# Optimization experiments

Measured on AMD Instinct MI355X. Metric: run time of the kernel, lower is better.

The kernel has to match this reference:

```python
import jax, jax.numpy as jnp
import numpy as np

D_MODEL = 512
N_HEADS = 8
HEAD_DIM = D_MODEL // N_HEADS
B, L, S = 4, 2048, 2048


def setup_inputs() -> dict:
    key = jax.random.key(0)
    ks = jax.random.split(key, 16)
    std = 1.0 / np.sqrt(D_MODEL)
    inp = {
        'queries': jax.random.normal(ks[0], (B, L, D_MODEL), jnp.float32),
        'keys': jax.random.normal(ks[1], (B, S, D_MODEL), jnp.float32),
        'values': jax.random.normal(ks[2], (B, S, D_MODEL), jnp.float32),
        'tau': jax.random.uniform(ks[3], (B,), jnp.float32, 0.5, 1.5),
        'delta': jax.random.normal(ks[4], (B,), jnp.float32) * 0.1,
        'Wq': jax.random.normal(ks[5], (D_MODEL, D_MODEL), jnp.float32) * std,
        'bq': jnp.zeros((D_MODEL,), jnp.float32),
        'Wk': jax.random.normal(ks[6], (D_MODEL, D_MODEL), jnp.float32) * std,
        'bk': jnp.zeros((D_MODEL,), jnp.float32),
        'Wv': jax.random.normal(ks[7], (D_MODEL, D_MODEL), jnp.float32) * std,
        'bv': jnp.zeros((D_MODEL,), jnp.float32),
        'Wo': jax.random.normal(ks[8], (D_MODEL, D_MODEL), jnp.float32) * std,
        'bo': jnp.zeros((D_MODEL,), jnp.float32),
    }
    return inp


def reference(queries, keys, values, tau, delta, Wq, bq, Wk, bk, Wv, bv, Wo, bo):
    Bq, Lq, _ = queries.shape
    Sk = keys.shape[1]
    H, E = N_HEADS, HEAD_DIM
    # projections -> [B, L, H, E]
    q = (queries @ Wq + bq).reshape(Bq, Lq, H, E)
    k = (keys @ Wk + bk).reshape(Bq, Sk, H, E)
    v = (values @ Wv + bv).reshape(Bq, Sk, H, E)
    scale = 1.0 / jnp.sqrt(jnp.float32(E))
    # scores: [B, H, L, S]
    scores = jnp.einsum('blhe,bshe->bhls', q, k)
    scores = scores * tau[:, None, None, None] + delta[:, None, None, None]
    A = jax.nn.softmax(scale * scores, axis=-1)  # dropout is identity in eval
    out = jnp.einsum('bhls,bshd->blhd', A, v).reshape(Bq, Lq, H * E)
    return out @ Wo + bo
```

## Files before the change

### kernel.cpp

```cpp
#include <hip/hip_runtime.h>
#include <stdint.h>

#define NB 4
#define LQ 2048
#define DM 512
#define NH 8
#define EH 64
#define MT (NB*LQ)
#define QBLK 128

typedef __attribute__((ext_vector_type(4)))  float f32x4;
typedef __attribute__((ext_vector_type(8)))  __bf16 bf16x8;
typedef __attribute__((ext_vector_type(8)))  unsigned short u16x8;
typedef __attribute__((ext_vector_type(4)))  float float4_t;
typedef __attribute__((ext_vector_type(2)))  unsigned int u32x2;

static __device__ __forceinline__ unsigned short f2bf(float f) {
  unsigned int u = __builtin_bit_cast(unsigned int, f);
  u += 0x7fffu + ((u >> 16) & 1u);
  return (unsigned short)(u >> 16);
}

static __device__ __forceinline__ void gload16(const void* g, void* l) {
  __builtin_amdgcn_global_load_lds(
      (__attribute__((address_space(1))) unsigned int*)(g),
      (__attribute__((address_space(3))) unsigned int*)(l), 16, 0, 0);
}

static __device__ __forceinline__ unsigned int cvt_pk_bf16(float lo, float hi) {
  unsigned int r;
  asm("v_cvt_pk_bf16_f32 %0, %1, %2" : "=v"(r) : "v"(lo), "v"(hi));
  return r;
}

extern "C" __global__ __launch_bounds__(256) void k_cast_x(
    const float* __restrict__ q, const float* __restrict__ k,
    const float* __restrict__ v, unsigned short* __restrict__ x) {
  int z = blockIdx.y;
  const float* src = (z == 0) ? q : ((z == 1) ? k : v);
  unsigned short* dst = x + (size_t)z * MT * DM;
  size_t i = ((size_t)blockIdx.x * 256 + threadIdx.x) * 8;
  float4_t a = *(const float4_t*)(src + i);
  float4_t b = *(const float4_t*)(src + i + 4);
  u16x8 r;
  r[0]=f2bf(a[0]); r[1]=f2bf(a[1]); r[2]=f2bf(a[2]); r[3]=f2bf(a[3]);
  r[4]=f2bf(b[0]); r[5]=f2bf(b[1]); r[6]=f2bf(b[2]); r[7]=f2bf(b[3]);
  *(u16x8*)(dst + i) = r;
}

extern "C" __global__ __launch_bounds__(256) void k_cast_wt(
    const float* __restrict__ wq, const float* __restrict__ wk,
    const float* __restrict__ wv, const float* __restrict__ wo,
    unsigned short* __restrict__ wt) {
  __shared__ float tile[64][65];
  int z = blockIdx.z;
  const float* w = (z==0)?wq : (z==1)?wk : (z==2)?wv : wo;
  unsigned short* dst = wt + (size_t)z * DM * DM;
  int kb = blockIdx.y * 64, nb = blockIdx.x * 64;
  int t = threadIdx.x;
  int r = t >> 2, c0 = (t & 3) * 16;
  #pragma unroll
  for (int i = 0; i < 16; i += 4) {
    float4_t v4 = *(const float4_t*)(w + (size_t)(kb + r) * DM + nb + c0 + i);
    tile[r][c0+i]   = v4[0]; tile[r][c0+i+1] = v4[1];
    tile[r][c0+i+2] = v4[2]; tile[r][c0+i+3] = v4[3];
  }
  __syncthreads();
  u16x8 o0, o1;
  #pragma unroll
  for (int i = 0; i < 8; ++i) o0[i] = f2bf(tile[c0+i][r]);
  #pragma unroll
  for (int i = 0; i < 8; ++i) o1[i] = f2bf(tile[c0+8+i][r]);
  *(u16x8*)(dst + (size_t)(nb + r) * DM + kb + c0)     = o0;
  *(u16x8*)(dst + (size_t)(nb + r) * DM + kb + c0 + 8) = o1;
}

extern "C" __global__ __launch_bounds__(256) void k_gemm_qkv(
    const unsigned short* __restrict__ X, const unsigned short* __restrict__ WT,
    const float* __restrict__ bq, const float* __restrict__ bk,
    const float* __restrict__ bv, unsigned short* __restrict__ out) {
  int z = blockIdx.z;
  const unsigned short* A  = X  + (size_t)z * MT * DM;
  const unsigned short* Bt = WT + (size_t)z * DM * DM;
  const float* bias = (z==0)?bq : (z==1)?bk : bv;
  unsigned short* dst = out + (size_t)z * MT * DM;

  __shared__ unsigned short As[2][128][32];
  __shared__ unsigned short Bs[2][128][32];

  int m0 = blockIdx.y * 128;
  int n0 = blockIdx.x * 128;
  int t = threadIdx.x;
  int lane = t & 63;
  int w = t >> 6;
  int wr = w >> 1, wc = w & 1;
  int g = lane >> 4, r15 = lane & 15;

  f32x4 acc[4][4];
  #pragma unroll
  for (int i=0;i<4;i++)
    #pragma unroll
    for (int j=0;j<4;j++)
      #pragma unroll
      for (int e=0;e<4;e++) acc[i][j][e] = 0.f;

  auto stage = [&](int bb, int kt) {
    int k0 = kt * 32;
    int sblk = (t & 3) ^ ((t >> 3) & 3);
    #pragma unroll
    for (int j=0;j<2;j++) {
      int o = t*16 + j*4096;
      int row = o >> 6;
      gload16(A  + (size_t)(m0+row)*DM + k0 + sblk*8, (char*)(&As[bb][0][0]) + o);
      gload16(Bt + (size_t)(n0+row)*DM + k0 + sblk*8, (char*)(&Bs[bb][0][0]) + o);
    }
  };

  stage(0, 0);
  __syncthreads();
  int buf = 0;
  for (int kt = 0; kt < DM/32; ++kt) {
    if (kt + 1 < DM/32) stage(buf ^ 1, kt + 1);
    bf16x8 af[4], bfr[4];
    #pragma unroll
    for (int mi=0;mi<4;mi++) {
      int row = wr*64 + mi*16 + r15;
      int blk = g ^ ((row >> 1) & 3);
      af[mi] = *(const bf16x8*)(&As[buf][row][blk*8]);
    }
    #pragma unroll
    for (int ni=0;ni<4;ni++) {
      int row = wc*64 + ni*16 + r15;
      int blk = g ^ ((row >> 1) & 3);
      bfr[ni] = *(const bf16x8*)(&Bs[buf][row][blk*8]);
    }
    #pragma unroll
    for (int mi=0;mi<4;mi++)
      #pragma unroll
      for (int ni=0;ni<4;ni++)
        acc[mi][ni] = __builtin_amdgcn_mfma_f32_16x16x32_bf16(af[mi], bfr[ni], acc[mi][ni], 0, 0, 0);
    __syncthreads();
    buf ^= 1;
  }
  #pragma unroll
  for (int ni=0;ni<4;ni++) {
    int n = n0 + wc*64 + ni*16 + r15;
    float bia = bias[n];
    int h = n >> 6, e = n & 63;
    #pragma unroll
    for (int mi=0;mi<4;mi++) {
      #pragma unroll
      for (int rg=0;rg<4;rg++) {
        int m = m0 + wr*64 + mi*16 + g*4 + rg;
        int b = m >> 11, s = m & 2047;
        dst[((size_t)((b*NH + h)*LQ + s))*EH + e] = f2bf(acc[mi][ni][rg] + bia);
      }
    }
  }
}

extern "C" __global__ __launch_bounds__(256) void k_vt(
    const unsigned short* __restrict__ qkv, unsigned short* __restrict__ vtg) {
  __shared__ unsigned short tile[64][65];
  int bh = blockIdx.y;
  int s0 = blockIdx.x * 64;
  const unsigned short* Vh = qkv + (size_t)2*MT*DM + (size_t)bh*LQ*EH;
  unsigned short* Ot = vtg + (size_t)bh*EH*LQ;
  int t = threadIdx.x;
  int r = t >> 2, c0 = (t & 3) * 16;
  u16x8 a = *(const u16x8*)(Vh + (size_t)(s0 + r)*EH + c0);
  u16x8 b = *(const u16x8*)(Vh + (size_t)(s0 + r)*EH + c0 + 8);
  #pragma unroll
  for (int i=0;i<8;i++) { tile[r][c0+i] = a[i]; tile[r][c0+8+i] = b[i]; }
  __syncthreads();
  u16x8 o0, o1;
  #pragma unroll
  for (int i=0;i<8;i++) o0[i] = tile[c0+i][r];
  #pragma unroll
  for (int i=0;i<8;i++) o1[i] = tile[c0+8+i][r];
  *(u16x8*)(Ot + (size_t)r*LQ + s0 + c0)     = o0;
  *(u16x8*)(Ot + (size_t)r*LQ + s0 + c0 + 8) = o1;
}

template<int NSPLIT>
__global__ __launch_bounds__(256, 4) void k_flash(
    const unsigned short* __restrict__ qkv, const unsigned short* __restrict__ vtg,
    const float* __restrict__ tau, unsigned short* __restrict__ aout,
    float* __restrict__ opart, float* __restrict__ lpart) {
  constexpr int SKV = LQ / NSPLIT;
  constexpr int NIT = SKV / 32;
  constexpr int CPX = (512 * NSPLIT) / 8;
  int bid = blockIdx.x;
  int wgid = (bid & 7) * CPX + (bid >> 3);
  int half = wgid % NSPLIT;
  int rest = wgid / NSPLIT;
  int qblk = rest & 15;
  int bh = rest >> 4;
  int batch = bh >> 3, h = bh & 7;

  const unsigned short* Qh  = qkv + (size_t)bh * LQ * EH + (size_t)qblk * QBLK * EH;
  const unsigned short* Kh  = qkv + (size_t)MT * DM + (size_t)bh * LQ * EH + (size_t)half * SKV * EH;
  const unsigned short* VTh = vtg + (size_t)bh * EH * LQ + (size_t)half * SKV;

  __shared__ unsigned short Ks[2][32][64];
  __shared__ unsigned short Vt[2][64][32];
  __shared__ unsigned short Pall[4][32][40];

  int t = threadIdx.x;
  int lane = t & 63;
  int wv = t >> 6;
  int q4 = lane & 15;
  int g  = lane >> 4;
  float C2 = tau[batch] * 0.18033688011112042f;

  unsigned short (*Pw)[40] = Pall[wv];

  auto stage = [&](int bb, int it) {
    int o = t * 16;
    int krow = t >> 3;
    int sblk = (t & 7) ^ ((krow ^ (krow >> 3)) & 7);
    gload16(Kh + (size_t)(it*32 + krow)*EH + sblk*8, (char*)(&Ks[bb][0][0]) + o);
    gload16(VTh + (size_t)(t >> 2)*LQ + it*32 + (t & 3)*8, (char*)(&Vt[bb][0][0]) + o);
  };

  bf16x8 qf[2][2];
  #pragma unroll
  for (int qt=0;qt<2;qt++)
    #pragma unroll
    for (int st=0;st<2;st++)
      qf[qt][st] = *(const bf16x8*)(Qh + (size_t)(wv*32 + qt*16 + q4)*EH + st*32 + g*8);

  stage(0, 0);

  const f32x4 Z4 = {0.f, 0.f, 0.f, 0.f};
  f32x4 oacc[4][2];
  #pragma unroll
  for (int a=0;a<4;a++)
    #pragma unroll
    for (int b2=0;b2<2;b2++)
      #pragma unroll
      for (int e=0;e<4;e++) oacc[a][b2][e] = 0.f;
  float lsp[2] = {0.f, 0.f};

  __syncthreads();
  int buf = 0;
  for (int it = 0; it < NIT; ++it) {
    if (it + 1 < NIT) stage(buf ^ 1, it + 1);

    f32x4 sac[2][2];
    __builtin_amdgcn_s_setprio(1);
    #pragma unroll
    for (int kvt=0; kvt<2; ++kvt) {
      int row = kvt*16 + q4;
      int S = (row ^ (row >> 3)) & 7;
      bf16x8 kf0 = *(const bf16x8*)(&Ks[buf][row][(g ^ S)*8]);
      sac[kvt][0] = __builtin_amdgcn_mfma_f32_16x16x32_bf16(kf0, qf[0][0], Z4, 0,0,0);
      sac[kvt][1] = __builtin_amdgcn_mfma_f32_16x16x32_bf16(kf0, qf[1][0], Z4, 0,0,0);
    }
    #pragma unroll
    for (int kvt=0; kvt<2; ++kvt) {
      int row = kvt*16 + q4;
      int S = (row ^ (row >> 3)) & 7;
      bf16x8 kf1 = *(const bf16x8*)(&Ks[buf][row][((4 + g) ^ S)*8]);
      sac[kvt][0] = __builtin_amdgcn_mfma_f32_16x16x32_bf16(kf1, qf[0][1], sac[kvt][0], 0,0,0);
      sac[kvt][1] = __builtin_amdgcn_mfma_f32_16x16x32_bf16(kf1, qf[1][1], sac[kvt][1], 0,0,0);
    }
    __builtin_amdgcn_s_setprio(0);

    #pragma unroll
    for (int qt=0; qt<2; ++qt) {
      int qrow = qt*16 + q4;
      #pragma unroll
      for (int kvt=0; kvt<2; ++kvt) {
        float p0 = __builtin_amdgcn_exp2f(sac[kvt][qt][0] * C2);
        float p1 = __builtin_amdgcn_exp2f(sac[kvt][qt][1] * C2);
        float p2 = __builtin_amdgcn_exp2f(sac[kvt][qt][2] * C2);
        float p3 = __builtin_amdgcn_exp2f(sac[kvt][qt][3] * C2);
        lsp[qt] += (p0 + p1) + (p2 + p3);
        u32x2 wpk;
        wpk[0] = cvt_pk_bf16(p0, p1);
        wpk[1] = cvt_pk_bf16(p2, p3);
        *(u32x2*)(&Pw[qrow][kvt*16 + g*4]) = wpk;
      }
    }
    asm volatile("s_waitcnt lgkmcnt(0)" ::: "memory");
    __builtin_amdgcn_sched_barrier(0);

    bf16x8 pf[2];
    #pragma unroll
    for (int qt=0; qt<2; ++qt)
      pf[qt] = *(const bf16x8*)(&Pw[qt*16 + q4][g*8]);
    __builtin_amdgcn_s_setprio(1);
    #pragma unroll
    for (int et=0; et<4; ++et) {
      bf16x8 vf = *(const bf16x8*)(&Vt[buf][et*16 + q4][g*8]);
      oacc[et][0] = __builtin_amdgcn_mfma_f32_16x16x32_bf16(vf, pf[0], oacc[et][0], 0,0,0);
      oacc[et][1] = __builtin_amdgcn_mfma_f32_16x16x32_bf16(vf, pf[1], oacc[et][1], 0,0,0);
    }
    __builtin_amdgcn_s_setprio(0);

    __syncthreads();
    buf ^= 1;
  }

  #pragma unroll
  for (int qt=0; qt<2; ++qt) {
    float s = lsp[qt];
    s += __shfl_xor(s, 16, 64);
    s += __shfl_xor(s, 32, 64);
    int q = qblk*QBLK + wv*32 + qt*16 + q4;
    if constexpr (NSPLIT == 1) {
      float inv = 1.f / s;
      unsigned short* rowp = aout + (size_t)(batch*LQ + q)*DM + h*EH;
      #pragma unroll
      for (int et=0; et<4; ++et) {
        #pragma unroll
        for (int rg=0; rg<4; rg+=2) {
          int e = et*16 + g*4 + rg;
          *(unsigned int*)(rowp + e) = cvt_pk_bf16(oacc[et][qt][rg] * inv, oacc[et][qt][rg+1] * inv);
        }
      }
    } else {
      size_t r = (size_t)bh * LQ + q;
      float* od = opart + (r*NSPLIT + half) * 64;
      #pragma unroll
      for (int et=0; et<4; ++et)
        *(float4_t*)(od + et*16 + g*4) = oacc[et][qt];
      if (g == 0) lpart[r*NSPLIT + half] = s;
    }
  }
}

extern "C" __global__ __launch_bounds__(256) void k_red(
    const float* __restrict__ op, const float* __restrict__ lp,
    unsigned short* __restrict__ aout) {
  int t = threadIdx.x;
  int r = blockIdx.x * 16 + (t >> 4);
  int e0 = (t & 15) * 4;
  float4_t a = *(const float4_t*)(op + ((size_t)r*2)*64 + e0);
  float4_t b = *(const float4_t*)(op + ((size_t)r*2 + 1)*64 + e0);
  float inv = 1.f / (lp[(size_t)r*2] + lp[(size_t)r*2 + 1]);
  int bh = r >> 11, q = r & 2047, batch = bh >> 3, h = bh & 7;
  unsigned short* dst = aout + (size_t)(batch*LQ + q)*DM + h*EH + e0;
  u32x2 w;
  w[0] = cvt_pk_bf16((a[0]+b[0])*inv, (a[1]+b[1])*inv);
  w[1] = cvt_pk_bf16((a[2]+b[2])*inv, (a[3]+b[3])*inv);
  *(u32x2*)dst = w;
}

extern "C" __global__ __launch_bounds__(256) void k_gemm_out(
    const unsigned short* __restrict__ A, const unsigned short* __restrict__ WT,
    const float* __restrict__ bo, float* __restrict__ out) {
  const unsigned short* Bt = WT + (size_t)3 * DM * DM;

  __shared__ unsigned short As[2][128][32];
  __shared__ unsigned short Bs[2][128][32];

  int m0 = blockIdx.y * 128;
  int n0 = blockIdx.x * 128;
  int t = threadIdx.x;
  int lane = t & 63;
  int w = t >> 6;
  int wr = w >> 1, wc = w & 1;
  int g = lane >> 4, r15 = lane & 15;

  f32x4 acc[4][4];
  #pragma unroll
  for (int i=0;i<4;i++)
    #pragma unroll
    for (int j=0;j<4;j++)
      #pragma unroll
      for (int e=0;e<4;e++) acc[i][j][e] = 0.f;

  auto stage = [&](int bb, int kt) {
    int k0 = kt * 32;
    int sblk = (t & 3) ^ ((t >> 3) & 3);
    #pragma unroll
    for (int j=0;j<2;j++) {
      int o = t*16 + j*4096;
      int row = o >> 6;
      gload16(A  + (size_t)(m0+row)*DM + k0 + sblk*8, (char*)(&As[bb][0][0]) + o);
      gload16(Bt + (size_t)(n0+row)*DM + k0 + sblk*8, (char*)(&Bs[bb][0][0]) + o);
    }
  };

  stage(0, 0);
  __syncthreads();
  int buf = 0;
  for (int kt = 0; kt < DM/32; ++kt) {
    if (kt + 1 < DM/32) stage(buf ^ 1, kt + 1);
    bf16x8 af[4], bfr[4];
    #pragma unroll
    for (int mi=0;mi<4;mi++) {
      int row = wr*64 + mi*16 + r15;
      int blk = g ^ ((row >> 1) & 3);
      af[mi] = *(const bf16x8*)(&As[buf][row][blk*8]);
    }
    #pragma unroll
    for (int ni=0;ni<4;ni++) {
      int row = wc*64 + ni*16 + r15;
      int blk = g ^ ((row >> 1) & 3);
      bfr[ni] = *(const bf16x8*)(&Bs[buf][row][blk*8]);
    }
    #pragma unroll
    for (int mi=0;mi<4;mi++)
      #pragma unroll
      for (int ni=0;ni<4;ni++)
        acc[mi][ni] = __builtin_amdgcn_mfma_f32_16x16x32_bf16(af[mi], bfr[ni], acc[mi][ni], 0, 0, 0);
    __syncthreads();
    buf ^= 1;
  }
  #pragma unroll
  for (int ni=0;ni<4;ni++) {
    int n = n0 + wc*64 + ni*16 + r15;
    float bia = bo[n];
    #pragma unroll
    for (int mi=0;mi<4;mi++) {
      #pragma unroll
      for (int rg=0;rg<4;rg++) {
        int m = m0 + wr*64 + mi*16 + g*4 + rg;
        out[(size_t)m*DM + n] = acc[mi][ni][rg] + bia;
      }
    }
  }
}

extern "C" void kernel_launch(void* const* d_in, const int* in_sizes, int n_in,
                              void* d_out, int out_size, void* d_ws, size_t ws_size,
                              hipStream_t stream) {
  const float* queries = (const float*)d_in[0];
  const float* keys    = (const float*)d_in[1];
  const float* values  = (const float*)d_in[2];
  const float* tau     = (const float*)d_in[3];
  const float* Wq = (const float*)d_in[5];
  const float* bq = (const float*)d_in[6];
  const float* Wk = (const float*)d_in[7];
  const float* bk = (const float*)d_in[8];
  const float* Wv = (const float*)d_in[9];
  const float* bv = (const float*)d_in[10];
  const float* Wo = (const float*)d_in[11];
  const float* bo = (const float*)d_in[12];
  float* out = (float*)d_out;

  char* ws = (char*)d_ws;
  unsigned short* WT   = (unsigned short*)(ws);
  unsigned short* X    = (unsigned short*)(ws + (2u  << 20));
  unsigned short* VTg  = (unsigned short*)(ws + (2u  << 20));
  unsigned short* AOut = (unsigned short*)(ws + (10u << 20));
  unsigned short* QKV  = (unsigned short*)(ws + (26u << 20));
  float*          Opart= (float*)(ws + (50u << 20));
  float*          Lpart= (float*)(ws + (84u << 20));

  k_cast_x  <<<dim3(2048, 3), dim3(256), 0, stream>>>(queries, keys, values, X);
  k_cast_wt <<<dim3(8, 8, 4), dim3(256), 0, stream>>>(Wq, Wk, Wv, Wo, WT);
  k_gemm_qkv<<<dim3(4, 64, 3), dim3(256), 0, stream>>>(X, WT, bq, bk, bv, QKV);
  k_vt      <<<dim3(32, 32), dim3(256), 0, stream>>>(QKV, VTg);

  if (ws_size >= ((size_t)85u << 20)) {
    k_flash<2><<<dim3(1024), dim3(256), 0, stream>>>(QKV, VTg, tau, AOut, Opart, Lpart);
    k_red    <<<dim3(4096), dim3(256), 0, stream>>>(Opart, Lpart, AOut);
  } else {
    k_flash<1><<<dim3(512), dim3(256), 0, stream>>>(QKV, VTg, tau, AOut, Opart, Lpart);
  }
  k_gemm_out<<<dim3(4, 64), dim3(256), 0, stream>>>(AOut, WT, bo, out);
}
```

Measured before the change: 118.2 us.

## Split KV four ways, fold tau scale into Q, compute row sums via MFMA

The tau*scale*log2e factor moves into the Q projection epilogue, so the flash kernel feeds raw scores to exp2. Row sums now come from an extra MFMA against a ones vector instead of scalar adds and shuffles. The KV split goes from 2 to 4 with 2048 blocks, partial outputs are stored as bf16 to halve traffic, and launch bounds rise to 6 waves per SIMD. The costs are lower precision in the partials and Q, more reduction work, and possible register spills from the higher occupancy target.

```diff
diff --git a/kernel.cpp b/kernel.cpp
--- a/kernel.cpp
+++ b/kernel.cpp
@@ -19,6 +19,11 @@
   unsigned int u = __builtin_bit_cast(unsigned int, f);
   u += 0x7fffu + ((u >> 16) & 1u);
   return (unsigned short)(u >> 16);
+}
+
+static __device__ __forceinline__ float bf2f(unsigned short h) {
+  unsigned int u = ((unsigned int)h) << 16;
+  return __builtin_bit_cast(float, u);
 }
 
 static __device__ __forceinline__ void gload16(const void* g, void* l) {
@@ -78,7 +83,8 @@
 extern "C" __global__ __launch_bounds__(256) void k_gemm_qkv(
     const unsigned short* __restrict__ X, const unsigned short* __restrict__ WT,
     const float* __restrict__ bq, const float* __restrict__ bk,
-    const float* __restrict__ bv, unsigned short* __restrict__ out) {
+    const float* __restrict__ bv, const float* __restrict__ tau,
+    unsigned short* __restrict__ out) {
   int z = blockIdx.z;
   const unsigned short* A  = X  + (size_t)z * MT * DM;
   const unsigned short* Bt = WT + (size_t)z * DM * DM;
@@ -90,6 +96,7 @@
 
   int m0 = blockIdx.y * 128;
   int n0 = blockIdx.x * 128;
+  float qsc = (z == 0) ? tau[m0 >> 11] * 0.18033688011112042f : 1.0f;
   int t = threadIdx.x;
   int lane = t & 63;
   int w = t >> 6;
@@ -153,7 +160,7 @@
       for (int rg=0;rg<4;rg++) {
         int m = m0 + wr*64 + mi*16 + g*4 + rg;
         int b = m >> 11, s = m & 2047;
-        dst[((size_t)((b*NH + h)*LQ + s))*EH + e] = f2bf(acc[mi][ni][rg] + bia);
+        dst[((size_t)((b*NH + h)*LQ + s))*EH + e] = f2bf((acc[mi][ni][rg] + bia) * qsc);
       }
     }
   }
@@ -183,24 +190,24 @@
 }
 
 template<int NSPLIT>
-__global__ __launch_bounds__(256, 4) void k_flash(
+__global__ __launch_bounds__(256, 6) void k_flash(
     const unsigned short* __restrict__ qkv, const unsigned short* __restrict__ vtg,
-    const float* __restrict__ tau, unsigned short* __restrict__ aout,
-    float* __restrict__ opart, float* __restrict__ lpart) {
+    unsigned short* __restrict__ aout,
+    unsigned short* __restrict__ opart, float* __restrict__ lpart) {
   constexpr int SKV = LQ / NSPLIT;
   constexpr int NIT = SKV / 32;
   constexpr int CPX = (512 * NSPLIT) / 8;
   int bid = blockIdx.x;
   int wgid = (bid & 7) * CPX + (bid >> 3);
-  int half = wgid % NSPLIT;
+  int part = wgid % NSPLIT;
   int rest = wgid / NSPLIT;
   int qblk = rest & 15;
   int bh = rest >> 4;
   int batch = bh >> 3, h = bh & 7;
 
   const unsigned short* Qh  = qkv + (size_t)bh * LQ * EH + (size_t)qblk * QBLK * EH;
-  const unsigned short* Kh  = qkv + (size_t)MT * DM + (size_t)bh * LQ * EH + (size_t)half * SKV * EH;
-  const unsigned short* VTh = vtg + (size_t)bh * EH * LQ + (size_t)half * SKV;
+  const unsigned short* Kh  = qkv + (size_t)MT * DM + (size_t)bh * LQ * EH + (size_t)part * SKV * EH;
+  const unsigned short* VTh = vtg + (size_t)bh * EH * LQ + (size_t)part * SKV;
 
   __shared__ unsigned short Ks[2][32][64];
   __shared__ unsigned short Vt[2][64][32];
@@ -211,7 +218,6 @@
   int wv = t >> 6;
   int q4 = lane & 15;
   int g  = lane >> 4;
-  float C2 = tau[batch] * 0.18033688011112042f;
 
   unsigned short (*Pw)[40] = Pall[wv];
 
@@ -232,6 +238,11 @@
 
   stage(0, 0);
 
+  union { unsigned short u[8]; bf16x8 v; } onesu;
+  #pragma unroll
+  for (int i=0;i<8;i++) onesu.u[i] = 0x3F80;
+  const bf16x8 ones8 = onesu.v;
+
   const f32x4 Z4 = {0.f, 0.f, 0.f, 0.f};
   f32x4 oacc[4][2];
   #pragma unroll
@@ -240,7 +251,11 @@
     for (int b2=0;b2<2;b2++)
       #pragma unroll
       for (int e=0;e<4;e++) oacc[a][b2][e] = 0.f;
-  float lsp[2] = {0.f, 0.f};
+  f32x4 ols[2];
+  #pragma unroll
+  for (int b2=0;b2<2;b2++)
+    #pragma unroll
+    for (int e=0;e<4;e++) ols[b2][e] = 0.f;
 
   __syncthreads();
   int buf = 0;
@@ -272,11 +287,10 @@
       int qrow = qt*16 + q4;
       #pragma unroll
       for (int kvt=0; kvt<2; ++kvt) {
-        float p0 = __builtin_amdgcn_exp2f(sac[kvt][qt][0] * C2);
-        float p1 = __builtin_amdgcn_exp2f(sac[kvt][qt][1] * C2);
-        float p2 = __builtin_amdgcn_exp2f(sac[kvt][qt][2] * C2);
-        float p3 = __builtin_amdgcn_exp2f(sac[kvt][qt][3] * C2);
-        lsp[qt] += (p0 + p1) + (p2 + p3);
+        float p0 = __builtin_amdgcn_exp2f(sac[kvt][qt][0]);
+        float p1 = __builtin_amdgcn_exp2f(sac[kvt][qt][1]);
+        float p2 = __builtin_amdgcn_exp2f(sac[kvt][qt][2]);
+        float p3 = __builtin_amdgcn_exp2f(sac[kvt][qt][3]);
         u32x2 wpk;
         wpk[0] = cvt_pk_bf16(p0, p1);
         wpk[1] = cvt_pk_bf16(p2, p3);
@@ -297,6 +311,8 @@
       oacc[et][0] = __builtin_amdgcn_mfma_f32_16x16x32_bf16(vf, pf[0], oacc[et][0], 0,0,0);
       oacc[et][1] = __builtin_amdgcn_mfma_f32_16x16x32_bf16(vf, pf[1], oacc[et][1], 0,0,0);
     }
+    ols[0] = __builtin_amdgcn_mfma_f32_16x16x32_bf16(ones8, pf[0], ols[0], 0,0,0);
+    ols[1] = __builtin_amdgcn_mfma_f32_16x16x32_bf16(ones8, pf[1], ols[1], 0,0,0);
     __builtin_amdgcn_s_setprio(0);
 
     __syncthreads();
@@ -305,9 +321,7 @@
 
   #pragma unroll
   for (int qt=0; qt<2; ++qt) {
-    float s = lsp[qt];
-    s += __shfl_xor(s, 16, 64);
-    s += __shfl_xor(s, 32, 64);
+    float s = ols[qt][0];
     int q = qblk*QBLK + wv*32 + qt*16 + q4;
     if constexpr (NSPLIT == 1) {
       float inv = 1.f / s;
@@ -322,29 +336,41 @@
       }
     } else {
       size_t r = (size_t)bh * LQ + q;
-      float* od = opart + (r*NSPLIT + half) * 64;
-      #pragma unroll
-      for (int et=0; et<4; ++et)
-        *(float4_t*)(od + et*16 + g*4) = oacc[et][qt];
-      if (g == 0) lpart[r*NSPLIT + half] = s;
+      unsigned short* od = opart + ((size_t)r*NSPLIT + part) * 64;
+      #pragma unroll
+      for (int et=0; et<4; ++et) {
+        u32x2 wpk;
+        wpk[0] = cvt_pk_bf16(oacc[et][qt][0], oacc[et][qt][1]);
+        wpk[1] = cvt_pk_bf16(oacc[et][qt][2], oacc[et][qt][3]);
+        *(u32x2*)(od + et*16 + g*4) = wpk;
+      }
+      if (g == 0) lpart[r*NSPLIT + part] = s;
     }
   }
 }
 
 extern "C" __global__ __launch_bounds__(256) void k_red(
-    const float* __restrict__ op, const float* __restrict__ lp,
+    const unsigned short* __restrict__ op, const float* __restrict__ lp,
     unsigned short* __restrict__ aout) {
   int t = threadIdx.x;
   int r = blockIdx.x * 16 + (t >> 4);
   int e0 = (t & 15) * 4;
-  float4_t a = *(const float4_t*)(op + ((size_t)r*2)*64 + e0);
-  float4_t b = *(const float4_t*)(op + ((size_t)r*2 + 1)*64 + e0);
-  float inv = 1.f / (lp[(size_t)r*2] + lp[(size_t)r*2 + 1]);
+  float acc0 = 0.f, acc1 = 0.f, acc2 = 0.f, acc3 = 0.f, ls = 0.f;
+  #pragma unroll
+  for (int qq = 0; qq < 4; ++qq) {
+    u32x2 wv = *(const u32x2*)(op + ((size_t)r*4 + qq)*64 + e0);
+    acc0 += bf2f((unsigned short)(wv[0] & 0xFFFF));
+    acc1 += bf2f((unsigned short)(wv[0] >> 16));
+    acc2 += bf2f((unsigned short)(wv[1] & 0xFFFF));
+    acc3 += bf2f((unsigned short)(wv[1] >> 16));
+    ls += lp[(size_t)r*4 + qq];
+  }
+  float inv = 1.f / ls;
   int bh = r >> 11, q = r & 2047, batch = bh >> 3, h = bh & 7;
   unsigned short* dst = aout + (size_t)(batch*LQ + q)*DM + h*EH + e0;
   u32x2 w;
-  w[0] = cvt_pk_bf16((a[0]+b[0])*inv, (a[1]+b[1])*inv);
-  w[1] = cvt_pk_bf16((a[2]+b[2])*inv, (a[3]+b[3])*inv);
+  w[0] = cvt_pk_bf16(acc0 * inv, acc1 * inv);
+  w[1] = cvt_pk_bf16(acc2 * inv, acc3 * inv);
   *(u32x2*)dst = w;
 }
 
@@ -448,19 +474,19 @@
   unsigned short* VTg  = (unsigned short*)(ws + (2u  << 20));
   unsigned short* AOut = (unsigned short*)(ws + (10u << 20));
   unsigned short* QKV  = (unsigned short*)(ws + (26u << 20));
-  float*          Opart= (float*)(ws + (50u << 20));
+  unsigned short* Opart= (unsigned short*)(ws + (50u << 20));
   float*          Lpart= (float*)(ws + (84u << 20));
 
   k_cast_x  <<<dim3(2048, 3), dim3(256), 0, stream>>>(queries, keys, values, X);
   k_cast_wt <<<dim3(8, 8, 4), dim3(256), 0, stream>>>(Wq, Wk, Wv, Wo, WT);
-  k_gemm_qkv<<<dim3(4, 64, 3), dim3(256), 0, stream>>>(X, WT, bq, bk, bv, QKV);
+  k_gemm_qkv<<<dim3(4, 64, 3), dim3(256), 0, stream>>>(X, WT, bq, bk, bv, tau, QKV);
   k_vt      <<<dim3(32, 32), dim3(256), 0, stream>>>(QKV, VTg);
 
   if (ws_size >= ((size_t)85u << 20)) {
-    k_flash<2><<<dim3(1024), dim3(256), 0, stream>>>(QKV, VTg, tau, AOut, Opart, Lpart);
+    k_flash<4><<<dim3(2048), dim3(256), 0, stream>>>(QKV, VTg, AOut, Opart, Lpart);
     k_red    <<<dim3(4096), dim3(256), 0, stream>>>(Opart, Lpart, AOut);
   } else {
-    k_flash<1><<<dim3(512), dim3(256), 0, stream>>>(QKV, VTg, tau, AOut, Opart, Lpart);
+    k_flash<1><<<dim3(512), dim3(256), 0, stream>>>(QKV, VTg, AOut, Opart, Lpart);
   }
   k_gemm_out<<<dim3(4, 64), dim3(256), 0, stream>>>(AOut, WT, bo, out);
 }
```

Result: slower. 166.5 us (+40.8%).
